# Kernel optimization log

Hardware: AMD Instinct MI355X
Metric: run time of the kernel (lower is better)

## Reference

```python
import jax, jax.numpy as jnp
import numpy as np

D_MODEL = 1024
N_HEADS = 16
D_K = D_MODEL // N_HEADS
ROPE_THETA = 10000.0
SOFT_CAP = 50.0  # Gemma-2-style logit soft cap
B, S = 4, 2048


def _rope(x, pos, theta=ROPE_THETA):
    # x: [..., S, d_k], interleaved-pair rotation
    d_k = x.shape[-1]
    inv_freq = theta ** (-jnp.arange(0, d_k, 2, dtype=jnp.float32) / d_k)  # [d_k/2]
    ang = pos.astype(jnp.float32)[:, None] * inv_freq[None, :]             # [S, d_k/2]
    cos, sin = jnp.cos(ang), jnp.sin(ang)
    x1, x2 = x[..., 0::2], x[..., 1::2]
    out_even = x1 * cos - x2 * sin
    out_odd = x1 * sin + x2 * cos
    return jnp.stack([out_even, out_odd], axis=-1).reshape(x.shape)


def setup_inputs() -> dict:
    key = jax.random.key(0)
    kx, kqkv, kout = jax.random.split(key, 3)
    scale = D_MODEL ** -0.5
    x = jax.random.normal(kx, (B, S, D_MODEL), dtype=jnp.float32)
    w_qkv = jax.random.normal(kqkv, (3 * D_MODEL, D_MODEL), dtype=jnp.float32) * scale
    w_out = jax.random.normal(kout, (D_MODEL, D_MODEL), dtype=jnp.float32) * scale
    return {"x": x, "w_qkv": w_qkv, "w_out": w_out}


def reference(x, w_qkv, w_out):
    b, s, d = x.shape
    # fused QKV projection (Linear, no bias): [B,S,3D]
    qkv = jnp.einsum('bsd,ed->bse', x, w_qkv)
    # '(n h d_k)' split -> [3, B, H, S, d_k]
    qkv = qkv.reshape(b, s, 3, N_HEADS, D_K)
    qkv = jnp.transpose(qkv, (2, 0, 3, 1, 4))
    q, k, v = qkv[0], qkv[1], qkv[2]
    pos = jnp.arange(s)
    q = _rope(q, pos)
    k = _rope(k, pos)
    scores = jnp.einsum('bhqd,bhkd->bhqk', q, k) / jnp.float32(D_K) ** 0.5
    scores = SOFT_CAP * jnp.tanh(scores / SOFT_CAP)  # cap_logits
    causal = jnp.tril(jnp.ones((s, s), dtype=bool))
    scores = jnp.where(causal, scores, jnp.float32(-1e30))
    attn = jax.nn.softmax(scores, axis=-1)
    out = jnp.einsum('bhqk,bhkd->bhqd', attn, v)
    out = jnp.transpose(out, (0, 2, 1, 3)).reshape(b, s, d)  # (h d_v) merge
    return jnp.einsum('bsd,ed->bse', out, w_out)
```

## Files before the change

kernel.cpp:

```cpp
#include <hip/hip_runtime.h>
#include <stdint.h>

#define S_LEN 2048
#define NH    16
#define DK    64
#define DM    1024

typedef __attribute__((ext_vector_type(8))) __bf16 bf16x8;
typedef __attribute__((ext_vector_type(8))) unsigned short u16x8;
typedef __attribute__((ext_vector_type(4))) float  f32x4;

static __device__ __forceinline__ unsigned short f2bf(float f) {
    union { float f; unsigned int u; } v; v.f = f;
    unsigned int r = v.u + 0x7FFFu + ((v.u >> 16) & 1u);
    return (unsigned short)(r >> 16);
}

static __device__ __forceinline__ float cap_exp2(float sp) {
    float u = exp2f(sp);
    float w = __builtin_amdgcn_rcpf(u + 1.0f);
    return exp2f(__builtin_fmaf(w, -144.2695040888f, 72.1347520444f));
}

#define GLL(src_, dst_) __builtin_amdgcn_global_load_lds(                              \
    (const __attribute__((address_space(1))) unsigned int*)(src_),                     \
    (__attribute__((address_space(3))) unsigned int*)(dst_), 16, 0, 0)

__global__ void detect_f32(const unsigned short* __restrict__ x, int* __restrict__ flag)
{
    __shared__ int tot;
    if (threadIdx.x == 0) tot = 0;
    __syncthreads();
    int weird = 0;
    for (int i = threadIdx.x; i < 16384; i += 256) {
        int e = (x[i] >> 7) & 0xFF;
        if (e == 0 || e < 87 || e > 167) weird++;
    }
    atomicAdd(&tot, weird);
    __syncthreads();
    if (threadIdx.x == 0) *flag = (tot > 4000) ? 1 : 0;
}

__global__ __launch_bounds__(256) void norm_bf16(const void* __restrict__ src,
                                                 unsigned short* __restrict__ dst,
                                                 int n, const int* __restrict__ flag)
{
    const int isf32 = *flag;
    int i = (blockIdx.x * 256 + threadIdx.x) * 8;
    if (i >= n) return;
    if (isf32) {
        const float* p = (const float*)src + i;
        u16x8 o;
        o[0] = f2bf(p[0]); o[1] = f2bf(p[1]); o[2] = f2bf(p[2]); o[3] = f2bf(p[3]);
        o[4] = f2bf(p[4]); o[5] = f2bf(p[5]); o[6] = f2bf(p[6]); o[7] = f2bf(p[7]);
        *(u16x8*)&dst[i] = o;
    } else {
        *(uint4*)&dst[i] = *(const uint4*)((const unsigned short*)src + i);
    }
}

__global__ __launch_bounds__(256) void rope_tab(float2* __restrict__ tab)
{
    int e = blockIdx.x * 256 + threadIdx.x;
    int s = e >> 5, d2 = e & 31;
    float invf = exp2f(-(float)d2 * 0.41524101186f);
    float sn, cs;
    sincosf((float)s * invf, &sn, &cs);
    tab[e] = make_float2(cs, sn);
}

#define VST  136

#define MFMA(a, b, c) __builtin_amdgcn_mfma_f32_16x16x32_bf16((a), (b), (c), 0, 0, 0)

#define GEMM_MAIN(Aptr, Wptr, lda_, ldw_)                                              \
    f32x4 zz = {0.f, 0.f, 0.f, 0.f};                                                   \
    f32x4 c00=zz,c01=zz,c02=zz,c03=zz, c10=zz,c11=zz,c12=zz,c13=zz,                    \
          c20=zz,c21=zz,c22=zz,c23=zz, c30=zz,c31=zz,c32=zz,c33=zz;                    \
    const int strow_ = wave * 16 + (lane >> 2);                                        \
    const int sgr_   = (((lane & 3) ^ ((strow_ >> 1) & 3))) << 3;                      \
    const unsigned short* Ag_ = (Aptr) + (size_t)(m0 + strow_) * (lda_) + sgr_;        \
    const unsigned short* Bg_ = (Wptr) + (size_t)(n0 + strow_) * (ldw_) + sgr_;        \
    unsigned short* Asw_ = As + wave * 512;                                            \
    unsigned short* Bsw_ = Bs + wave * 512;                                            \
    const int kfG_ = ((quad ^ ((l16 >> 1) & 3))) << 3;                                 \
    for (int k0 = 0; k0 < 1024; k0 += 32) {                                            \
        __syncthreads();                                                               \
        GLL(Ag_ + k0,                     Asw_);                                       \
        GLL(Ag_ + k0 + 64 * (size_t)(lda_), Asw_ + 2048);                              \
        GLL(Bg_ + k0,                     Bsw_);                                       \
        GLL(Bg_ + k0 + 64 * (size_t)(ldw_), Bsw_ + 2048);                              \
        asm volatile("s_waitcnt vmcnt(0)" ::: "memory");                               \
        __syncthreads();                                                               \
        bf16x8 a0 = *(const bf16x8*)&As[(wm +  0 + l16) * 32 + kfG_];                  \
        bf16x8 a1 = *(const bf16x8*)&As[(wm + 16 + l16) * 32 + kfG_];                  \
        bf16x8 a2 = *(const bf16x8*)&As[(wm + 32 + l16) * 32 + kfG_];                  \
        bf16x8 a3 = *(const bf16x8*)&As[(wm + 48 + l16) * 32 + kfG_];                  \
        bf16x8 b0 = *(const bf16x8*)&Bs[(wn +  0 + l16) * 32 + kfG_];                  \
        bf16x8 b1 = *(const bf16x8*)&Bs[(wn + 16 + l16) * 32 + kfG_];                  \
        bf16x8 b2 = *(const bf16x8*)&Bs[(wn + 32 + l16) * 32 + kfG_];                  \
        bf16x8 b3 = *(const bf16x8*)&Bs[(wn + 48 + l16) * 32 + kfG_];                  \
        c00 = MFMA(a0, b0, c00); c01 = MFMA(a0, b1, c01);                              \
        c02 = MFMA(a0, b2, c02); c03 = MFMA(a0, b3, c03);                              \
        c10 = MFMA(a1, b0, c10); c11 = MFMA(a1, b1, c11);                              \
        c12 = MFMA(a1, b2, c12); c13 = MFMA(a1, b3, c13);                              \
        c20 = MFMA(a2, b0, c20); c21 = MFMA(a2, b1, c21);                              \
        c22 = MFMA(a2, b2, c22); c23 = MFMA(a2, b3, c23);                              \
        c30 = MFMA(a3, b0, c30); c31 = MFMA(a3, b1, c31);                              \
        c32 = MFMA(a3, b2, c32); c33 = MFMA(a3, b3, c33);                              \
    }

__global__ __launch_bounds__(256) void gemm_fused(const unsigned short* __restrict__ A,
                                                  const unsigned short* __restrict__ W,
                                                  const float2* __restrict__ tab,
                                                  unsigned short* __restrict__ qr,
                                                  unsigned short* __restrict__ kr,
                                                  unsigned short* __restrict__ vt)
{
    __shared__ __align__(16) unsigned short smem[128 * VST];
    unsigned short* As = smem;
    unsigned short* Bs = smem + 4096;

    const int tid  = threadIdx.x;
    const int wave = tid >> 6;
    const int lane = tid & 63;
    const int quad = lane >> 4;
    const int l16  = lane & 15;
    const int m0 = blockIdx.y * 128;
    const int n0 = blockIdx.x * 128;
    const int wm = (wave >> 1) * 64;
    const int wn = (wave & 1) * 64;

    GEMM_MAIN(A, W, 1024, 1024)

    const int cls = n0 >> 10;
    if (cls < 2) {
        unsigned short* dst = cls ? kr : qr;
        const float qs = cls ? 1.0f : 0.125f * 0.0577078016f;

#define ROPE_R(accv, MTc, rc, even_, h_, d_) do {                                      \
        int row = m0 + wm + (MTc) * 16 + quad * 4 + (rc);                              \
        int s = row & (S_LEN - 1), b = row >> 11;                                      \
        float2 cssn = tab[(s << 5) + ((d_) >> 1)];                                     \
        float own = accv[rc];                                                          \
        float oth = __shfl_xor(own, 1);                                                \
        float res = (even_) ? (own * cssn.x - oth * cssn.y)                            \
                            : (oth * cssn.y + own * cssn.x);                           \
        dst[((size_t)(b * NH + (h_)) * S_LEN + s) * DK + (d_)] = f2bf(res * qs);       \
    } while (0)

#define ROPE_ST(accv, MTc, NTc) do {                                                   \
        int col = (n0 & 1023) + wn + (NTc) * 16 + l16;                                 \
        int h = col >> 6, d = col & 63;                                                \
        int even = !(d & 1);                                                           \
        ROPE_R(accv, MTc, 0, even, h, d);                                              \
        ROPE_R(accv, MTc, 1, even, h, d);                                              \
        ROPE_R(accv, MTc, 2, even, h, d);                                              \
        ROPE_R(accv, MTc, 3, even, h, d);                                              \
    } while (0)

        ROPE_ST(c00, 0, 0); ROPE_ST(c01, 0, 1); ROPE_ST(c02, 0, 2); ROPE_ST(c03, 0, 3);
        ROPE_ST(c10, 1, 0); ROPE_ST(c11, 1, 1); ROPE_ST(c12, 1, 2); ROPE_ST(c13, 1, 3);
        ROPE_ST(c20, 2, 0); ROPE_ST(c21, 2, 1); ROPE_ST(c22, 2, 2); ROPE_ST(c23, 2, 3);
        ROPE_ST(c30, 3, 0); ROPE_ST(c31, 3, 1); ROPE_ST(c32, 3, 2); ROPE_ST(c33, 3, 3);
    } else {
        __syncthreads();

#define VST_ACC(accv, MTc, NTc) do {                                                   \
        int dl = wn + (NTc) * 16 + l16;                                                \
        int base = dl * VST + wm + (MTc) * 16 + quad * 4;                              \
        smem[base + 0] = f2bf(accv[0]); smem[base + 1] = f2bf(accv[1]);                \
        smem[base + 2] = f2bf(accv[2]); smem[base + 3] = f2bf(accv[3]);                \
    } while (0)

        VST_ACC(c00, 0, 0); VST_ACC(c01, 0, 1); VST_ACC(c02, 0, 2); VST_ACC(c03, 0, 3);
        VST_ACC(c10, 1, 0); VST_ACC(c11, 1, 1); VST_ACC(c12, 1, 2); VST_ACC(c13, 1, 3);
        VST_ACC(c20, 2, 0); VST_ACC(c21, 2, 1); VST_ACC(c22, 2, 2); VST_ACC(c23, 2, 3);
        VST_ACC(c30, 3, 0); VST_ACC(c31, 3, 1); VST_ACC(c32, 3, 2); VST_ACC(c33, 3, 3);
        __syncthreads();
        int dl = tid >> 1, sh = (tid & 1) * 64;
        int vcol = (n0 - 2048) + dl;
        int h = vcol >> 6, dd = vcol & 63;
        int b = m0 >> 11, s0 = m0 & (S_LEN - 1);
        unsigned short* dst = vt + (((size_t)(b * NH + h) * DK + dd) * S_LEN + s0 + sh);
        const unsigned short* src = smem + dl * VST + sh;
#pragma unroll
        for (int i = 0; i < 64; i += 8)
            *(bf16x8*)&dst[i] = *(const bf16x8*)&src[i];
    }
}

__global__ __launch_bounds__(256) void gemm_out(const unsigned short* __restrict__ A,
                                                const unsigned short* __restrict__ W,
                                                float* __restrict__ C)
{
    __shared__ __align__(16) unsigned short As[4096];
    __shared__ __align__(16) unsigned short Bs[4096];
    const int tid  = threadIdx.x;
    const int wave = tid >> 6;
    const int lane = tid & 63;
    const int quad = lane >> 4;
    const int l16  = lane & 15;
    const int m0 = blockIdx.y * 128;
    const int n0 = blockIdx.x * 128;
    const int wm = (wave >> 1) * 64;
    const int wn = (wave & 1) * 64;

    GEMM_MAIN(A, W, 1024, 1024)

#define OUT_ST(accv, MTc, NTc) do {                                                    \
    int col = n0 + wn + (NTc) * 16 + l16;                                              \
    int rowb = m0 + wm + (MTc) * 16 + quad * 4;                                        \
    C[(size_t)(rowb + 0) * 1024 + col] = accv[0];                                      \
    C[(size_t)(rowb + 1) * 1024 + col] = accv[1];                                      \
    C[(size_t)(rowb + 2) * 1024 + col] = accv[2];                                      \
    C[(size_t)(rowb + 3) * 1024 + col] = accv[3];                                      \
} while (0)

    OUT_ST(c00, 0, 0); OUT_ST(c01, 0, 1); OUT_ST(c02, 0, 2); OUT_ST(c03, 0, 3);
    OUT_ST(c10, 1, 0); OUT_ST(c11, 1, 1); OUT_ST(c12, 1, 2); OUT_ST(c13, 1, 3);
    OUT_ST(c20, 2, 0); OUT_ST(c21, 2, 1); OUT_ST(c22, 2, 2); OUT_ST(c23, 2, 3);
    OUT_ST(c30, 3, 0); OUT_ST(c31, 3, 1); OUT_ST(c32, 3, 2); OUT_ST(c33, 3, 3);
}

#define PPL 72

__global__ __launch_bounds__(256) void attn_fwd(const unsigned short* __restrict__ qr,
                                                const unsigned short* __restrict__ kr,
                                                const unsigned short* __restrict__ vt,
                                                unsigned short* __restrict__ aout)
{
    __shared__ __align__(16) unsigned short kvs[2][2][4096];
    __shared__ __align__(16) unsigned short plds[4][16 * PPL];
    int blk  = blockIdx.x;
    int pr   = blk & 15;
    int bh   = blk >> 4;
    int b    = bh >> 4, h = bh & 15;
    int wave = threadIdx.x >> 6;
    int lane = threadIdx.x & 63;
    int quad = lane >> 4, l16 = lane & 15;

    const unsigned short* kbase = kr + (size_t)bh * S_LEN * DK;
    const unsigned short* vbase = vt + (size_t)bh * DK * S_LEN;
    unsigned short* pw = &plds[wave][0];

    u16x8 onesu = {0x3F80,0x3F80,0x3F80,0x3F80,0x3F80,0x3F80,0x3F80,0x3F80};
    bf16x8 vones = *(bf16x8*)&onesu;

    const int lam3  = lane >> 3;
    const int sc3p  = (lane & 7) ^ lam3;
    const int strow = wave * 8 + lam3;
    const int stcol = sc3p * 8;
    const int kfA = l16 * 64 + ((quad ^ (l16 & 7)) << 3);

#define STAGE(c_, nb_) do {                                                            \
    const int j0s = (c_) * 64;                                                         \
    unsigned short* kd = &kvs[nb_][0][wave * 512];                                     \
    unsigned short* vd = &kvs[nb_][1][wave * 512];                                     \
    const unsigned short* kg = kbase + (size_t)(j0s + strow) * 64 + stcol;             \
    const unsigned short* vg = vbase + (size_t)strow * S_LEN + j0s + stcol;            \
    GLL(kg, kd); GLL(kg + 32 * 64, kd + 2048);                                         \
    GLL(vg, vd); GLL(vg + 32 * S_LEN, vd + 2048);                                      \
} while (0)

#define QK_LDS(kb_) do {                                                               \
    bf16x8 ka, kb;                                                                     \
    ka = *(const bf16x8*)&(kb_)[kfA];          kb = *(const bf16x8*)&(kb_)[kfA ^ 32];  \
    sc0 = MFMA(qf0, ka, sc0); sc0 = MFMA(qf1, kb, sc0);                                \
    ka = *(const bf16x8*)&(kb_)[kfA + 1024];   kb = *(const bf16x8*)&(kb_)[(kfA + 1024) ^ 32]; \
    sc1 = MFMA(qf0, ka, sc1); sc1 = MFMA(qf1, kb, sc1);                                \
    ka = *(const bf16x8*)&(kb_)[kfA + 2048];   kb = *(const bf16x8*)&(kb_)[(kfA + 2048) ^ 32]; \
    sc2 = MFMA(qf0, ka, sc2); sc2 = MFMA(qf1, kb, sc2);                                \
    ka = *(const bf16x8*)&(kb_)[kfA + 3072];   kb = *(const bf16x8*)&(kb_)[(kfA + 3072) ^ 32]; \
    sc3 = MFMA(qf0, ka, sc3); sc3 = MFMA(qf1, kb, sc3);                                \
} while (0)

#define PV_LDS(vb_) do {                                                               \
    bf16x8 pf0 = *(const bf16x8*)&pw[l16 * PPL + quad * 8];                            \
    bf16x8 pf1 = *(const bf16x8*)&pw[l16 * PPL + 32 + quad * 8];                       \
    bf16x8 va, vb;                                                                     \
    va = *(const bf16x8*)&(vb_)[kfA];          vb = *(const bf16x8*)&(vb_)[kfA ^ 32];  \
    o0 = MFMA(pf0, va, o0); o0 = MFMA(pf1, vb, o0);                                    \
    va = *(const bf16x8*)&(vb_)[kfA + 1024];   vb = *(const bf16x8*)&(vb_)[(kfA + 1024) ^ 32]; \
    o1 = MFMA(pf0, va, o1); o1 = MFMA(pf1, vb, o1);                                    \
    va = *(const bf16x8*)&(vb_)[kfA + 2048];   vb = *(const bf16x8*)&(vb_)[(kfA + 2048) ^ 32]; \
    o2 = MFMA(pf0, va, o2); o2 = MFMA(pf1, vb, o2);                                    \
    va = *(const bf16x8*)&(vb_)[kfA + 3072];   vb = *(const bf16x8*)&(vb_)[(kfA + 3072) ^ 32]; \
    o3 = MFMA(pf0, va, o3); o3 = MFMA(pf1, vb, o3);                                    \
    o4 = MFMA(pf0, vones, o4); o4 = MFMA(pf1, vones, o4);                              \
} while (0)

#define P_STORE(rc, p0_, p1_, p2_, p3_) do {                                           \
    unsigned int r01, r23;                                                             \
    asm("v_cvt_pk_bf16_f32 %0, %1, %2" : "=v"(r01) : "v"(p0_), "v"(p1_));              \
    asm("v_cvt_pk_bf16_f32 %0, %1, %2" : "=v"(r23) : "v"(p2_), "v"(p3_));              \
    int rb = (quad * 4 + (rc)) * PPL + l16;                                            \
    pw[rb]      = (unsigned short)r01;                                                 \
    pw[rb + 16] = (unsigned short)(r01 >> 16);                                         \
    pw[rb + 32] = (unsigned short)r23;                                                 \
    pw[rb + 48] = (unsigned short)(r23 >> 16);                                         \
} while (0)

#define ROW_UPD_N(rc) do {                                                             \
    float p0 = cap_exp2(sc0[rc]);                                                      \
    float p1 = cap_exp2(sc1[rc]);                                                      \
    float p2 = cap_exp2(sc2[rc]);                                                      \
    float p3 = cap_exp2(sc3[rc]);                                                      \
    P_STORE(rc, p0, p1, p2, p3);                                                       \
} while (0)

#define ROW_UPD_M(rc) do {                                                             \
    int qrow = q0w + quad * 4 + (rc);                                                  \
    float p0 = (j0 + l16      > qrow) ? 0.f : cap_exp2(sc0[rc]);                       \
    float p1 = (j0 + 16 + l16 > qrow) ? 0.f : cap_exp2(sc1[rc]);                       \
    float p2 = (j0 + 32 + l16 > qrow) ? 0.f : cap_exp2(sc2[rc]);                       \
    float p3 = (j0 + 48 + l16 > qrow) ? 0.f : cap_exp2(sc3[rc]);                       \
    P_STORE(rc, p0, p1, p2, p3);                                                       \
} while (0)

    for (int side = 0; side < 2; ++side) {
        const int qblk = side ? (31 - pr) : pr;
        const int q0w  = qblk * 64 + wave * 16;

        const unsigned short* qbase = qr + ((size_t)bh * S_LEN + q0w) * DK;
        bf16x8 qf0 = *(const bf16x8*)&qbase[l16 * DK + quad * 8];
        bf16x8 qf1 = *(const bf16x8*)&qbase[l16 * DK + 32 + quad * 8];

        f32x4 zz = {0.f, 0.f, 0.f, 0.f};
        f32x4 o0 = zz, o1 = zz, o2 = zz, o3 = zz, o4 = zz;

        const int nch = qblk + 1;

        STAGE(0, 0);
        asm volatile("s_waitcnt vmcnt(0)" ::: "memory");
        __syncthreads();
        int cb = 0;

        for (int c = 0; c < nch - 1; ++c) {
            STAGE(c + 1, cb ^ 1);
            f32x4 sc0 = zz, sc1 = zz, sc2 = zz, sc3 = zz;
            QK_LDS(&kvs[cb][0][0]);
            ROW_UPD_N(0); ROW_UPD_N(1); ROW_UPD_N(2); ROW_UPD_N(3);
            asm volatile("s_waitcnt lgkmcnt(0)" ::: "memory");
            PV_LDS(&kvs[cb][1][0]);
            asm volatile("s_waitcnt vmcnt(0)" ::: "memory");
            __syncthreads();
            cb ^= 1;
        }

        {
            const int j0 = (nch - 1) * 64;
            f32x4 sc0 = zz, sc1 = zz, sc2 = zz, sc3 = zz;
            QK_LDS(&kvs[cb][0][0]);
            ROW_UPD_M(0); ROW_UPD_M(1); ROW_UPD_M(2); ROW_UPD_M(3);
            asm volatile("s_waitcnt lgkmcnt(0)" ::: "memory");
            PV_LDS(&kvs[cb][1][0]);
            __syncthreads();
        }

#define OUT_ROW(rc) do {                                                               \
        int qrow = q0w + quad * 4 + (rc);                                              \
        size_t off = (size_t)(b * S_LEN + qrow) * DM + h * DK + l16;                   \
        float rl = 1.0f / o4[rc];                                                      \
        aout[off +  0] = f2bf(o0[rc] * rl);                                            \
        aout[off + 16] = f2bf(o1[rc] * rl);                                            \
        aout[off + 32] = f2bf(o2[rc] * rl);                                            \
        aout[off + 48] = f2bf(o3[rc] * rl);                                            \
} while (0)

        OUT_ROW(0); OUT_ROW(1); OUT_ROW(2); OUT_ROW(3);
#undef OUT_ROW
    }
}

extern "C" void kernel_launch(void* const* d_in, const int* in_sizes, int n_in,
                              void* d_out, int out_size, void* d_ws, size_t ws_size,
                              hipStream_t stream)
{
    const void* x = nullptr; const void* wqkv = nullptr; const void* wout = nullptr;
    for (int i = 0; i < n_in; ++i) {
        if      (in_sizes[i] == 8388608) x    = d_in[i];
        else if (in_sizes[i] == 3145728) wqkv = d_in[i];
        else if (in_sizes[i] == 1048576) wout = d_in[i];
    }
    float* out = (float*)d_out;
    unsigned short* ws   = (unsigned short*)d_ws;
    unsigned short* ob16 = (unsigned short*)d_out;

    unsigned short* qr     = ws;
    unsigned short* kr     = ws + (size_t)8388608;
    unsigned short* aout   = ws + (size_t)16777216;
    int* flag              = (int*)(ws + (size_t)25165824);
    unsigned short* wqkvbf = aout;
    unsigned short* woutbf = qr;
    float2* tab            = (float2*)(ws + (size_t)16777216 + 4194304);

    unsigned short* vt  = ob16;
    unsigned short* xbf = ob16 + (size_t)8388608;

    detect_f32<<<1, 256, 0, stream>>>((const unsigned short*)x, flag);
    norm_bf16<<<4096, 256, 0, stream>>>(x, xbf, 8388608, flag);
    norm_bf16<<<1536, 256, 0, stream>>>(wqkv, wqkvbf, 3145728, flag);
    rope_tab<<<256, 256, 0, stream>>>(tab);
    gemm_fused<<<dim3(24, 64), 256, 0, stream>>>(xbf, wqkvbf, tab, qr, kr, vt);
    attn_fwd<<<1024, 256, 0, stream>>>(qr, kr, vt, aout);
    norm_bf16<<<512, 256, 0, stream>>>(wout, woutbf, 1048576, flag);
    gemm_out<<<dim3(8, 64), 256, 0, stream>>>(aout, woutbf, out);
}
```

Before: 340.0 us.

## Double-buffer LDS tiles in GEMM main loop to prefetch next K slice

Both projection GEMMs now keep two LDS buffers per operand. The next 32-wide K slice is loaded asynchronously while the MFMAs run on the current one, and there is one barrier per iteration instead of two. This is meant to hide global-to-LDS load latency behind MFMA work. The cost is double the LDS for the operand tiles in gemm_out, which could lower occupancy. The explicit vmcnt wait is gone, so correctness relies on the barrier draining the outstanding loads.

```diff
diff --git a/kernel.cpp b/kernel.cpp
--- a/kernel.cpp
+++ b/kernel.cpp
@@ -81,25 +81,34 @@
     const int sgr_   = (((lane & 3) ^ ((strow_ >> 1) & 3))) << 3;                      \
     const unsigned short* Ag_ = (Aptr) + (size_t)(m0 + strow_) * (lda_) + sgr_;        \
     const unsigned short* Bg_ = (Wptr) + (size_t)(n0 + strow_) * (ldw_) + sgr_;        \
-    unsigned short* Asw_ = As + wave * 512;                                            \
-    unsigned short* Bsw_ = Bs + wave * 512;                                            \
     const int kfG_ = ((quad ^ ((l16 >> 1) & 3))) << 3;                                 \
+    {                                                                                  \
+        unsigned short* Ad_ = As + wave * 512;                                         \
+        unsigned short* Bd_ = Bs + wave * 512;                                         \
+        GLL(Ag_, Ad_); GLL(Ag_ + 64 * (size_t)(lda_), Ad_ + 2048);                     \
+        GLL(Bg_, Bd_); GLL(Bg_ + 64 * (size_t)(ldw_), Bd_ + 2048);                     \
+    }                                                                                  \
+    __syncthreads();                                  \
+    int cbuf_ = 0;                                                                     \
     for (int k0 = 0; k0 < 1024; k0 += 32) {                                            \
-        __syncthreads();                                                               \
-        GLL(Ag_ + k0,                     Asw_);                                       \
-        GLL(Ag_ + k0 + 64 * (size_t)(lda_), Asw_ + 2048);                              \
-        GLL(Bg_ + k0,                     Bsw_);                                       \
-        GLL(Bg_ + k0 + 64 * (size_t)(ldw_), Bsw_ + 2048);                              \
-        asm volatile("s_waitcnt vmcnt(0)" ::: "memory");                               \
-        __syncthreads();                                                               \
-        bf16x8 a0 = *(const bf16x8*)&As[(wm +  0 + l16) * 32 + kfG_];                  \
-        bf16x8 a1 = *(const bf16x8*)&As[(wm + 16 + l16) * 32 + kfG_];                  \
-        bf16x8 a2 = *(const bf16x8*)&As[(wm + 32 + l16) * 32 + kfG_];                  \
-        bf16x8 a3 = *(const bf16x8*)&As[(wm + 48 + l16) * 32 + kfG_];                  \
-        bf16x8 b0 = *(const bf16x8*)&Bs[(wn +  0 + l16) * 32 + kfG_];                  \
-        bf16x8 b1 = *(const bf16x8*)&Bs[(wn + 16 + l16) * 32 + kfG_];                  \
-        bf16x8 b2 = *(const bf16x8*)&Bs[(wn + 32 + l16) * 32 + kfG_];                  \
-        bf16x8 b3 = *(const bf16x8*)&Bs[(wn + 48 + l16) * 32 + kfG_];                  \
+        if (k0 + 32 < 1024) {                                                          \
+            unsigned short* Ad_ = As + ((cbuf_ ^ 1) << 12) + wave * 512;               \
+            unsigned short* Bd_ = Bs + ((cbuf_ ^ 1) << 12) + wave * 512;               \
+            GLL(Ag_ + k0 + 32, Ad_);                                                   \
+            GLL(Ag_ + k0 + 32 + 64 * (size_t)(lda_), Ad_ + 2048);                      \
+            GLL(Bg_ + k0 + 32, Bd_);                                                   \
+            GLL(Bg_ + k0 + 32 + 64 * (size_t)(ldw_), Bd_ + 2048);                      \
+        }                                                                              \
+        const unsigned short* Ar_ = As + (cbuf_ << 12);                                \
+        const unsigned short* Br_ = Bs + (cbuf_ << 12);                                \
+        bf16x8 a0 = *(const bf16x8*)&Ar_[(wm +  0 + l16) * 32 + kfG_];                 \
+        bf16x8 a1 = *(const bf16x8*)&Ar_[(wm + 16 + l16) * 32 + kfG_];                 \
+        bf16x8 a2 = *(const bf16x8*)&Ar_[(wm + 32 + l16) * 32 + kfG_];                 \
+        bf16x8 a3 = *(const bf16x8*)&Ar_[(wm + 48 + l16) * 32 + kfG_];                 \
+        bf16x8 b0 = *(const bf16x8*)&Br_[(wn +  0 + l16) * 32 + kfG_];                 \
+        bf16x8 b1 = *(const bf16x8*)&Br_[(wn + 16 + l16) * 32 + kfG_];                 \
+        bf16x8 b2 = *(const bf16x8*)&Br_[(wn + 32 + l16) * 32 + kfG_];                 \
+        bf16x8 b3 = *(const bf16x8*)&Br_[(wn + 48 + l16) * 32 + kfG_];                 \
         c00 = MFMA(a0, b0, c00); c01 = MFMA(a0, b1, c01);                              \
         c02 = MFMA(a0, b2, c02); c03 = MFMA(a0, b3, c03);                              \
         c10 = MFMA(a1, b0, c10); c11 = MFMA(a1, b1, c11);                              \
@@ -108,6 +117,8 @@
         c22 = MFMA(a2, b2, c22); c23 = MFMA(a2, b3, c23);                              \
         c30 = MFMA(a3, b0, c30); c31 = MFMA(a3, b1, c31);                              \
         c32 = MFMA(a3, b2, c32); c33 = MFMA(a3, b3, c33);                              \
+        __syncthreads();                    \
+        cbuf_ ^= 1;                                                                    \
     }
 
 __global__ __launch_bounds__(256) void gemm_fused(const unsigned short* __restrict__ A,
@@ -119,7 +130,7 @@
 {
     __shared__ __align__(16) unsigned short smem[128 * VST];
     unsigned short* As = smem;
-    unsigned short* Bs = smem + 4096;
+    unsigned short* Bs = smem + 8192;
 
     const int tid  = threadIdx.x;
     const int wave = tid >> 6;
@@ -194,8 +205,8 @@
                                                 const unsigned short* __restrict__ W,
                                                 float* __restrict__ C)
 {
-    __shared__ __align__(16) unsigned short As[4096];
-    __shared__ __align__(16) unsigned short Bs[4096];
+    __shared__ __align__(16) unsigned short As[8192];
+    __shared__ __align__(16) unsigned short Bs[8192];
     const int tid  = threadIdx.x;
     const int wave = tid >> 6;
     const int lane = tid & 63;
```

New measurement: 327.4 us. -3.7%, faster.
